# Kernel tuning notes

Hardware: AMD Instinct MI355X
Metric: run time of the kernel (lower is better)

The kernel has to match this reference:

```python
import jax, jax.numpy as jnp
import numpy as np

B, N, D = 16, 1024, 768
H = 12
HS = D // H
L = 2  # n_ffn_layers
EPS = 1e-6


def layernorm(x, scale, bias):
    mu = jnp.mean(x, axis=-1, keepdims=True)
    var = jnp.var(x, axis=-1, keepdims=True)
    return (x - mu) * jax.lax.rsqrt(var + EPS) * scale + bias


def log_cosh(x):
    # numerically stable log(cosh(x)) = |x| + log1p(exp(-2|x|)) - log(2)
    ax = jnp.abs(x)
    return ax + jnp.log1p(jnp.exp(-2.0 * ax)) - jnp.log(2.0)


def setup_inputs() -> dict:
    key = jax.random.key(0)
    ks = jax.random.split(key, 8)
    x = jax.random.normal(ks[0], (B, N, D), dtype=jnp.float32)
    # pre-attention LayerNorm params
    ln1_scale = jnp.ones((D,), jnp.float32)
    ln1_bias = jnp.zeros((D,), jnp.float32)
    # per-head value projections [H, D, HS] (Dense, no bias)
    Wv = jax.random.normal(ks[1], (H, D, HS), jnp.float32) / np.sqrt(D)
    # per-head circulant rows alpha_delta [H, N], truncated_normal(stddev=sqrt(1/N))
    alpha = jax.random.truncated_normal(ks[2], -2.0, 2.0, (H, N), jnp.float32) * np.sqrt(1.0 / N)
    # FFN: L layers of Dense(D) + LayerNorm + swish
    Wf = jax.random.normal(ks[3], (L, D, D), jnp.float32) / np.sqrt(D)
    bf = jnp.zeros((L, D), jnp.float32)
    lnf_scale = jnp.ones((L, D), jnp.float32)
    lnf_bias = jnp.zeros((L, D), jnp.float32)
    return {"x": x, "ln1_scale": ln1_scale, "ln1_bias": ln1_bias, "Wv": Wv,
            "alpha": alpha, "Wf": Wf, "bf": bf,
            "lnf_scale": lnf_scale, "lnf_bias": lnf_bias}


def reference(x, ln1_scale, ln1_bias, Wv, alpha, Wf, bf, lnf_scale, lnf_bias):
    b, n, d = x.shape
    h, hs = Wv.shape[0], Wv.shape[2]
    # --- multi-head positional (circulant) attention on LN(x) ---
    xn = layernorm(x, ln1_scale, ln1_bias)
    v = jnp.einsum('bnd,hdk->bhnk', xn, Wv)  # per-head values
    # circulant matrix C[h, i, j] = alpha[h, (i - j) mod n]  (scipy.linalg.circulant)
    idx = (jnp.arange(n)[:, None] - jnp.arange(n)[None, :]) % n  # [n, n]
    C = alpha[:, idx]                                            # [h, n, n]
    y = jnp.einsum('hij,bhjk->bhik', C, v)                       # [b, h, n, hs]
    y = jnp.transpose(y, (0, 2, 1, 3)).reshape(b, n, h * hs)     # concat heads
    x = x + y
    # --- FFN: [Dense(D) -> LayerNorm -> swish] x L ---
    z = x
    for l in range(Wf.shape[0]):
        z = jax.nn.swish(layernorm(z @ Wf[l] + bf[l], lnf_scale[l], lnf_bias[l]))
    return log_cosh(z + x)
```

## Files before the change

### kernel.cpp

```cpp
#include <hip/hip_runtime.h>
#include <cstdint>
#include <cstddef>


typedef __attribute__((ext_vector_type(8))) short bf16x8;
typedef __attribute__((ext_vector_type(4))) float f32x4;
typedef __attribute__((ext_vector_type(4))) unsigned short us4;

__device__ __forceinline__ unsigned short f2bf(float f) {
  unsigned int u = __builtin_bit_cast(unsigned int, f);
  u += 0x7FFFu + ((u >> 16) & 1u);
  return (unsigned short)(u >> 16);
}
__device__ __forceinline__ float bf2f(unsigned short u) {
  return __builtin_bit_cast(float, (unsigned int)u << 16);
}

__device__ __forceinline__ void g2l16(const void* g, void* l) {
  __builtin_amdgcn_global_load_lds(
      (const __attribute__((address_space(1))) unsigned int*)g,
      (__attribute__((address_space(3))) unsigned int*)l,
      16, 0, 0);
}

#define WAITB(n) asm volatile("s_waitcnt vmcnt(" #n ") lgkmcnt(0)\n\ts_barrier" ::: "memory")

__global__ __launch_bounds__(256) void pack_w2t(const float* __restrict__ Wv,
                                                unsigned short* __restrict__ W2t) {
  int o = blockIdx.x * 256 + threadIdx.x;
  int np = o / 768, d = o - np * 768;
  int h = np >> 6, k = np & 63;
  W2t[o] = f2bf(Wv[h * 49152 + d * 64 + k]);
}

__global__ __launch_bounds__(256) void pack_wft(const float* __restrict__ Wf,
                                                unsigned short* __restrict__ Wft) {
  int o = blockIdx.x * 256 + threadIdx.x;
  int l = o / 589824, rem = o - l * 589824;
  int np = rem / 768, d = rem - np * 768;
  Wft[o] = f2bf(Wf[l * 589824 + d * 768 + np]);
}

__device__ __forceinline__ void wave_reduce2(float& s, float& s2) {
#pragma unroll
  for (int off = 32; off > 0; off >>= 1) {
    s += __shfl_down(s, off);
    s2 += __shfl_down(s2, off);
  }
  s = __shfl(s, 0);
  s2 = __shfl(s2, 0);
}

__global__ __launch_bounds__(256) void ln1_kernel(const float* __restrict__ x,
                                                  const float* __restrict__ sc,
                                                  const float* __restrict__ bi,
                                                  unsigned short* __restrict__ out) {
  int row = blockIdx.x * 4 + (threadIdx.x >> 6);
  int lane = threadIdx.x & 63;
  size_t base = (size_t)row * 768;
  float4 v[3];
#pragma unroll
  for (int j = 0; j < 3; ++j) v[j] = *(const float4*)(x + base + lane * 4 + j * 256);
  float s = 0.f, s2 = 0.f;
#pragma unroll
  for (int j = 0; j < 3; ++j) {
    s += v[j].x + v[j].y + v[j].z + v[j].w;
    s2 += v[j].x * v[j].x + v[j].y * v[j].y + v[j].z * v[j].z + v[j].w * v[j].w;
  }
  wave_reduce2(s, s2);
  float mu = s * (1.0f / 768.0f);
  float var = s2 * (1.0f / 768.0f) - mu * mu;
  float r = rsqrtf(var + 1e-6f);
#pragma unroll
  for (int j = 0; j < 3; ++j) {
    int d = lane * 4 + j * 256;
    float4 scv = *(const float4*)(sc + d);
    float4 biv = *(const float4*)(bi + d);
    us4 o;
    o[0] = f2bf((v[j].x - mu) * r * scv.x + biv.x);
    o[1] = f2bf((v[j].y - mu) * r * scv.y + biv.y);
    o[2] = f2bf((v[j].z - mu) * r * scv.z + biv.z);
    o[3] = f2bf((v[j].w - mu) * r * scv.w + biv.w);
    *(us4*)(out + base + d) = o;
  }
}

__global__ __launch_bounds__(256) void lnswish_kernel(const unsigned short* __restrict__ g,
                                                      const float* __restrict__ sc,
                                                      const float* __restrict__ bi,
                                                      unsigned short* __restrict__ out) {
  int row = blockIdx.x * 4 + (threadIdx.x >> 6);
  int lane = threadIdx.x & 63;
  size_t base = (size_t)row * 768;
  float v[3][4];
#pragma unroll
  for (int j = 0; j < 3; ++j) {
    us4 gv = *(const us4*)(g + base + lane * 4 + j * 256);
#pragma unroll
    for (int q = 0; q < 4; ++q) v[j][q] = bf2f(gv[q]);
  }
  float s = 0.f, s2 = 0.f;
#pragma unroll
  for (int j = 0; j < 3; ++j)
#pragma unroll
    for (int q = 0; q < 4; ++q) { s += v[j][q]; s2 += v[j][q] * v[j][q]; }
  wave_reduce2(s, s2);
  float mu = s * (1.0f / 768.0f);
  float var = s2 * (1.0f / 768.0f) - mu * mu;
  float r = rsqrtf(var + 1e-6f);
#pragma unroll
  for (int j = 0; j < 3; ++j) {
    int d = lane * 4 + j * 256;
    float4 scv = *(const float4*)(sc + d);
    float4 biv = *(const float4*)(bi + d);
    const float* scp = &scv.x;
    const float* bip = &biv.x;
    us4 o;
#pragma unroll
    for (int q = 0; q < 4; ++q) {
      float z = (v[j][q] - mu) * r * scp[q] + bip[q];
      o[q] = f2bf(z / (1.0f + __expf(-z)));
    }
    *(us4*)(out + base + d) = o;
  }
}

__global__ __launch_bounds__(256) void final_kernel(const unsigned short* __restrict__ g,
                                                    const float* __restrict__ sc,
                                                    const float* __restrict__ bi,
                                                    const unsigned short* __restrict__ x2,
                                                    float* __restrict__ out) {
  int row = blockIdx.x * 4 + (threadIdx.x >> 6);
  int lane = threadIdx.x & 63;
  size_t base = (size_t)row * 768;
  float v[3][4];
#pragma unroll
  for (int j = 0; j < 3; ++j) {
    us4 gv = *(const us4*)(g + base + lane * 4 + j * 256);
#pragma unroll
    for (int q = 0; q < 4; ++q) v[j][q] = bf2f(gv[q]);
  }
  float s = 0.f, s2 = 0.f;
#pragma unroll
  for (int j = 0; j < 3; ++j)
#pragma unroll
    for (int q = 0; q < 4; ++q) { s += v[j][q]; s2 += v[j][q] * v[j][q]; }
  wave_reduce2(s, s2);
  float mu = s * (1.0f / 768.0f);
  float var = s2 * (1.0f / 768.0f) - mu * mu;
  float r = rsqrtf(var + 1e-6f);
#pragma unroll
  for (int j = 0; j < 3; ++j) {
    int d = lane * 4 + j * 256;
    float4 scv = *(const float4*)(sc + d);
    float4 biv = *(const float4*)(bi + d);
    us4 xv = *(const us4*)(x2 + base + d);
    const float* scp = &scv.x;
    const float* bip = &biv.x;
    float4 o;
    float* op = &o.x;
#pragma unroll
    for (int q = 0; q < 4; ++q) {
      float z = (v[j][q] - mu) * r * scp[q] + bip[q];
      float sw = z / (1.0f + __expf(-z));
      float t = sw + bf2f(xv[q]);
      float ax = fabsf(t);
      op[q] = ax + __logf(1.0f + __expf(-2.0f * ax)) - 0.69314718055994531f;
    }
    *(float4*)(out + base + d) = o;
  }
}

__device__ __forceinline__ void gemm_core(const unsigned short* __restrict__ A,
                                          const unsigned short* __restrict__ Bt,
                                          int K, int m0, int n0,
                                          unsigned short* sA, unsigned short* sB,
                                          f32x4 acc[4][4]) {
  const int tid = threadIdx.x;
  const int wave = tid >> 6, lane = tid & 63;
  const int wm = (wave >> 1) << 6, wn = (wave & 1) << 6;
  const int fm = lane & 15, fq = lane >> 4;
  const int r0 = tid >> 2, r1 = r0 + 64;
  const int cg = tid & 3;
  const int cs0 = (cg ^ ((r0 >> 1) & 3)) << 3;
  const int cs1 = (cg ^ ((r1 >> 1) & 3)) << 3;
  const int ld0 = r0 * 32 + (cg << 3);
  const int ld1 = r1 * 32 + (cg << 3);
  const int niter = K >> 5;

#define STAGE(k0v, buf)                                                       \
  {                                                                           \
    unsigned short* dA = sA + (buf) * 4096;                                   \
    unsigned short* dB = sB + (buf) * 4096;                                   \
    g2l16(A + (size_t)(m0 + r0) * K + (k0v) + cs0, dA + ld0);                 \
    g2l16(Bt + (size_t)(n0 + r0) * K + (k0v) + cs0, dB + ld0);                \
    g2l16(A + (size_t)(m0 + r1) * K + (k0v) + cs1, dA + ld1);                 \
    g2l16(Bt + (size_t)(n0 + r1) * K + (k0v) + cs1, dB + ld1);                \
  }
#define GCOMP(bc)                                                             \
  {                                                                           \
    const unsigned short* pA = sA + (bc) * 4096;                              \
    const unsigned short* pB = sB + (bc) * 4096;                              \
    bf16x8 aq[4], bq[4];                                                      \
    _Pragma("unroll") for (int t = 0; t < 4; ++t) {                           \
      int ra = wm + (t << 4) + fm;                                            \
      int rb = wn + (t << 4) + fm;                                            \
      aq[t] = *(const bf16x8*)(pA + (ra << 5) + ((fq ^ ((ra >> 1) & 3)) << 3)); \
      bq[t] = *(const bf16x8*)(pB + (rb << 5) + ((fq ^ ((rb >> 1) & 3)) << 3)); \
    }                                                                         \
    _Pragma("unroll") for (int mt = 0; mt < 4; ++mt)                          \
    _Pragma("unroll") for (int nt = 0; nt < 4; ++nt)                          \
      acc[mt][nt] = __builtin_amdgcn_mfma_f32_16x16x32_bf16(aq[mt], bq[nt],   \
                                                            acc[mt][nt], 0, 0, 0); \
  }

  STAGE(0, 0);
  STAGE(32, 1);
  int bs = 2, bc = 0;
  for (int it = 0; it < niter - 1; ++it) {
    WAITB(4);
    if (it + 2 < niter) {
      STAGE((it + 2) << 5, bs);
      bs = (bs == 2) ? 0 : bs + 1;
    }
    GCOMP(bc);
    bc = (bc == 2) ? 0 : bc + 1;
  }
  WAITB(0);
  GCOMP(bc);
#undef STAGE
}

__device__ __forceinline__ void decode_mn_768(int f, int& m0, int& n0) {
  int xcd = f & 7, s = f >> 3;
  int g = s / 6, bx = s - g * 6;
  m0 = (xcd + g * 8) << 7;
  n0 = bx << 7;
}

__global__ __launch_bounds__(256, 3) void gemm1_kernel(const unsigned short* __restrict__ A,
                                                       const unsigned short* __restrict__ Bt,
                                                       unsigned short* __restrict__ Vt) {
  __shared__ unsigned short sA[3 * 4096];
  __shared__ unsigned short sB[3 * 4096];
  f32x4 acc[4][4] = {};
  int m0, n0;
  decode_mn_768(blockIdx.x, m0, n0);
  gemm_core(A, Bt, 768, m0, n0, sA, sB, acc);
  const int wave = threadIdx.x >> 6, lane = threadIdx.x & 63;
  const int wm = (wave >> 1) << 6, wn = (wave & 1) << 6;
  const int fm = lane & 15, fq = lane >> 4;
#pragma unroll
  for (int mt = 0; mt < 4; ++mt) {
    int rowb = m0 + wm + (mt << 4) + (fq << 2);
    int b = rowb >> 10, n = rowb & 1023;
#pragma unroll
    for (int nt = 0; nt < 4; ++nt) {
      int col = n0 + wn + (nt << 4) + fm;
      int h = col >> 6, ck = col & 63;
      size_t off = ((size_t)h << 20) + (size_t)((b << 6) + ck) * 1024 + n;
      us4 v;
#pragma unroll
      for (int r = 0; r < 4; ++r) v[r] = f2bf(acc[mt][nt][r]);
      *(us4*)(Vt + off) = v;
    }
  }
}

__global__ __launch_bounds__(256, 3) void circ_kernel(const float* __restrict__ alpha,
                                                      const unsigned short* __restrict__ Vt,
                                                      const float* __restrict__ xin,
                                                      unsigned short* __restrict__ x2bf) {
  __shared__ unsigned short sAc[8 * 1168];
  __shared__ unsigned short sB[4 * 4096];
  f32x4 acc[4][4] = {};
  int f = blockIdx.x;
  int xcd = f & 7, s = f >> 3;
  int h = s >> 3, t = s & 7;
  int mr = xcd >> 1, nr = xcd & 1;
  int m0 = ((mr << 1) + (t >> 2)) << 7;
  int n0 = ((nr << 2) + (t & 3)) << 7;

  const int tid = threadIdx.x;
  const int wave = tid >> 6, lane = tid & 63;
  const int wm = (wave >> 1) << 6, wn = (wave & 1) << 6;
  const int fm = lane & 15, fq = lane >> 4;

  const float* ah = alpha + (h << 10);
#pragma unroll
  for (int c = 0; c < 8; ++c)
    for (int u = tid; u < 1160; u += 256)
      sAc[c * 1168 + u] = f2bf(ah[(m0 - 897 - u - c) & 1023]);
  asm volatile("s_waitcnt vmcnt(0)" ::: "memory");

  const unsigned short* Bt = Vt + ((size_t)h << 20);
  const int r0 = tid >> 2, r1 = r0 + 64;
  const int cg = tid & 3;
  const int cs0 = (cg ^ ((r0 >> 1) & 3)) << 3;
  const int cs1 = (cg ^ ((r1 >> 1) & 3)) << 3;
  const int ld0 = r0 * 32 + (cg << 3);
  const int ld1 = r1 * 32 + (cg << 3);

#define STAGEB(k0v, buf)                                                      \
  {                                                                           \
    unsigned short* dB = sB + (buf) * 4096;                                   \
    g2l16(Bt + (size_t)(n0 + r0) * 1024 + (k0v) + cs0, dB + ld0);             \
    g2l16(Bt + (size_t)(n0 + r1) * 1024 + (k0v) + cs1, dB + ld1);             \
  }
#define CCOMP(it)                                                             \
  {                                                                           \
    const unsigned short* pB = sB + ((it) & 3) * 4096;                        \
    int k0v = (it) << 5;                                                      \
    bf16x8 aq[4], bq[4];                                                      \
    _Pragma("unroll") for (int t_ = 0; t_ < 4; ++t_) {                        \
      int rl = wm + (t_ << 4) + fm;                                           \
      int d = k0v + (fq << 3) + 127 - rl;                                     \
      int c = d & 7;                                                          \
      aq[t_] = *(const bf16x8*)(sAc + c * 1168 + (d - c));                    \
      int rb = wn + (t_ << 4) + fm;                                           \
      bq[t_] = *(const bf16x8*)(pB + (rb << 5) + ((fq ^ ((rb >> 1) & 3)) << 3)); \
    }                                                                         \
    _Pragma("unroll") for (int mt = 0; mt < 4; ++mt)                          \
    _Pragma("unroll") for (int nt = 0; nt < 4; ++nt)                          \
      acc[mt][nt] = __builtin_amdgcn_mfma_f32_16x16x32_bf16(aq[mt], bq[nt],   \
                                                            acc[mt][nt], 0, 0, 0); \
  }

  STAGEB(0, 0);
  STAGEB(32, 1);
  STAGEB(64, 2);
  for (int it = 0; it < 30; ++it) {
    WAITB(4);
    if (it < 29) STAGEB((it + 3) << 5, (it + 3) & 3);
    CCOMP(it);
  }
  WAITB(2);
  CCOMP(30);
  WAITB(0);
  CCOMP(31);
#undef STAGEB

#pragma unroll
  for (int mt = 0; mt < 4; ++mt) {
    int ib = m0 + wm + (mt << 4) + (fq << 2);
#pragma unroll
    for (int nt = 0; nt < 4; ++nt) {
      int c = n0 + wn + (nt << 4) + fm;
      int b = c >> 6, k = c & 63;
      size_t off = ((size_t)(b << 10) + ib) * 768 + (h << 6) + k;
#pragma unroll
      for (int r = 0; r < 4; ++r) {
        float val = acc[mt][nt][r] + xin[off + (size_t)r * 768];
        x2bf[off + (size_t)r * 768] = f2bf(val);
      }
    }
  }
}

__global__ __launch_bounds__(256, 3) void gemmf_kernel(const unsigned short* __restrict__ A,
                                                       const unsigned short* __restrict__ Bt,
                                                       const float* __restrict__ bias,
                                                       unsigned short* __restrict__ g) {
  __shared__ unsigned short sA[3 * 4096];
  __shared__ unsigned short sB[3 * 4096];
  f32x4 acc[4][4] = {};
  int m0, n0;
  decode_mn_768(blockIdx.x, m0, n0);
  gemm_core(A, Bt, 768, m0, n0, sA, sB, acc);
  const int wave = threadIdx.x >> 6, lane = threadIdx.x & 63;
  const int wm = (wave >> 1) << 6, wn = (wave & 1) << 6;
  const int fm = lane & 15, fq = lane >> 4;
#pragma unroll
  for (int mt = 0; mt < 4; ++mt) {
    int rowb = m0 + wm + (mt << 4) + (fq << 2);
#pragma unroll
    for (int nt = 0; nt < 4; ++nt) {
      int col = n0 + wn + (nt << 4) + fm;
      float bc = bias[col];
#pragma unroll
      for (int r = 0; r < 4; ++r)
        g[(size_t)(rowb + r) * 768 + col] = f2bf(acc[mt][nt][r] + bc);
    }
  }
}

extern "C" void kernel_launch(void* const* d_in, const int* in_sizes, int n_in,
                              void* d_out, int out_size, void* d_ws, size_t ws_size,
                              hipStream_t stream) {
  const float* x = (const float*)d_in[0];
  const float* ln1_s = (const float*)d_in[1];
  const float* ln1_b = (const float*)d_in[2];
  const float* Wv = (const float*)d_in[3];
  const float* alpha = (const float*)d_in[4];
  const float* Wf = (const float*)d_in[5];
  const float* bf = (const float*)d_in[6];
  const float* lnf_s = (const float*)d_in[7];
  const float* lnf_b = (const float*)d_in[8];
  float* out = (float*)d_out;

  char* ws = (char*)d_ws;
  unsigned short* slotA = (unsigned short*)ws;
  unsigned short* Vt = (unsigned short*)(ws + 25165824);
  unsigned short* gbf = Vt;
  unsigned short* slotX = (unsigned short*)(ws + 50331648);
  unsigned short* W2t = (unsigned short*)(ws + 75497472);
  unsigned short* Wft = (unsigned short*)(ws + 76677120);

  pack_w2t<<<2304, 256, 0, stream>>>(Wv, W2t);
  pack_wft<<<4608, 256, 0, stream>>>(Wf, Wft);

  ln1_kernel<<<4096, 256, 0, stream>>>(x, ln1_s, ln1_b, slotA);
  gemm1_kernel<<<768, 256, 0, stream>>>(slotA, W2t, Vt);
  circ_kernel<<<768, 256, 0, stream>>>(alpha, Vt, x, slotX);
  gemmf_kernel<<<768, 256, 0, stream>>>(slotX, Wft, bf, gbf);
  lnswish_kernel<<<4096, 256, 0, stream>>>(gbf, lnf_s, lnf_b, slotA);
  gemmf_kernel<<<768, 256, 0, stream>>>(slotA, Wft + 589824, bf + 768, gbf);
  final_kernel<<<4096, 256, 0, stream>>>(gbf, lnf_s + 768, lnf_b + 768, slotX, out);
}
```

Measured before the change: 282.6 us.

## Replace 128x128 GEMMs with 256x256-tile eight-wave MFMA GEMM using interleaved schedule

The three dense GEMMs (value projection and both FFN layers) move from 128x128 tiles with 4 waves to a 256x256 tile computed by 512 threads. Each K-step is 64 wide, with two LDS buffers in 128KB of dynamic shared memory. The main loop interleaves LDS fragment loads, partial global-to-LDS staging and MFMA quadrants with s_setprio and fine-grained barriers, to raise arithmetic intensity and hide load latency. The trade-off is that only 192 workgroups are launched, fewer than the CU count, and occupancy is limited by the large LDS footprint.

```diff
diff --git a/kernel.cpp b/kernel.cpp
--- a/kernel.cpp
+++ b/kernel.cpp
@@ -24,6 +24,8 @@
 }
 
 #define WAITB(n) asm volatile("s_waitcnt vmcnt(" #n ") lgkmcnt(0)\n\ts_barrier" ::: "memory")
+#define BARX asm volatile("s_waitcnt lgkmcnt(0)\n\ts_barrier" ::: "memory")
+#define BARV(n) asm volatile("s_waitcnt vmcnt(" #n ") lgkmcnt(0)\n\ts_barrier" ::: "memory")
 
 __global__ __launch_bounds__(256) void pack_w2t(const float* __restrict__ Wv,
                                                 unsigned short* __restrict__ W2t) {
@@ -171,98 +173,174 @@
   }
 }
 
-__device__ __forceinline__ void gemm_core(const unsigned short* __restrict__ A,
-                                          const unsigned short* __restrict__ Bt,
-                                          int K, int m0, int n0,
-                                          unsigned short* sA, unsigned short* sB,
-                                          f32x4 acc[4][4]) {
+template <int K>
+__device__ __forceinline__ void gemm256(const unsigned short* __restrict__ A,
+                                        const unsigned short* __restrict__ Bt,
+                                        int m0, int n0, unsigned short* lds,
+                                        f32x4 acc[8][4]) {
   const int tid = threadIdx.x;
-  const int wave = tid >> 6, lane = tid & 63;
-  const int wm = (wave >> 1) << 6, wn = (wave & 1) << 6;
+  const int lane = tid & 63;
+  const int wid = tid >> 6;
+  const int wm = (wid >> 2) << 6;
+  const int wn = (wid & 3) << 5;
   const int fm = lane & 15, fq = lane >> 4;
-  const int r0 = tid >> 2, r1 = r0 + 64;
-  const int cg = tid & 3;
-  const int cs0 = (cg ^ ((r0 >> 1) & 3)) << 3;
-  const int cs1 = (cg ^ ((r1 >> 1) & 3)) << 3;
-  const int ld0 = r0 * 32 + (cg << 3);
-  const int ld1 = r1 * 32 + (cg << 3);
-  const int niter = K >> 5;
-
-#define STAGE(k0v, buf)                                                       \
-  {                                                                           \
-    unsigned short* dA = sA + (buf) * 4096;                                   \
-    unsigned short* dB = sB + (buf) * 4096;                                   \
-    g2l16(A + (size_t)(m0 + r0) * K + (k0v) + cs0, dA + ld0);                 \
-    g2l16(Bt + (size_t)(n0 + r0) * K + (k0v) + cs0, dB + ld0);                \
-    g2l16(A + (size_t)(m0 + r1) * K + (k0v) + cs1, dA + ld1);                 \
-    g2l16(Bt + (size_t)(n0 + r1) * K + (k0v) + cs1, dB + ld1);                \
-  }
-#define GCOMP(bc)                                                             \
-  {                                                                           \
-    const unsigned short* pA = sA + (bc) * 4096;                              \
-    const unsigned short* pB = sB + (bc) * 4096;                              \
-    bf16x8 aq[4], bq[4];                                                      \
-    _Pragma("unroll") for (int t = 0; t < 4; ++t) {                           \
-      int ra = wm + (t << 4) + fm;                                            \
-      int rb = wn + (t << 4) + fm;                                            \
-      aq[t] = *(const bf16x8*)(pA + (ra << 5) + ((fq ^ ((ra >> 1) & 3)) << 3)); \
-      bq[t] = *(const bf16x8*)(pB + (rb << 5) + ((fq ^ ((rb >> 1) & 3)) << 3)); \
-    }                                                                         \
-    _Pragma("unroll") for (int mt = 0; mt < 4; ++mt)                          \
-    _Pragma("unroll") for (int nt = 0; nt < 4; ++nt)                          \
-      acc[mt][nt] = __builtin_amdgcn_mfma_f32_16x16x32_bf16(aq[mt], bq[nt],   \
-                                                            acc[mt][nt], 0, 0, 0); \
-  }
-
-  STAGE(0, 0);
-  STAGE(32, 1);
-  int bs = 2, bc = 0;
-  for (int it = 0; it < niter - 1; ++it) {
-    WAITB(4);
-    if (it + 2 < niter) {
-      STAGE((it + 2) << 5, bs);
-      bs = (bs == 2) ? 0 : bs + 1;
-    }
-    GCOMP(bc);
-    bc = (bc == 2) ? 0 : bc + 1;
-  }
-  WAITB(0);
-  GCOMP(bc);
-#undef STAGE
-}
-
-__device__ __forceinline__ void decode_mn_768(int f, int& m0, int& n0) {
-  int xcd = f & 7, s = f >> 3;
-  int g = s / 6, bx = s - g * 6;
-  m0 = (xcd + g * 8) << 7;
-  n0 = bx << 7;
-}
-
-__global__ __launch_bounds__(256, 3) void gemm1_kernel(const unsigned short* __restrict__ A,
-                                                       const unsigned short* __restrict__ Bt,
-                                                       unsigned short* __restrict__ Vt) {
-  __shared__ unsigned short sA[3 * 4096];
-  __shared__ unsigned short sB[3 * 4096];
-  f32x4 acc[4][4] = {};
+  const int srow = tid >> 3;
+  const int sslot = (tid & 7) ^ (srow & 7);
+  const size_t abase = (size_t)(m0 + srow) * K + (sslot << 3);
+  const size_t bbase = (size_t)(n0 + srow) * K + (sslot << 3);
+
+  bf16x8 aq[4][2], bq[4][2];
+
+#define STG_A(kt, bb, c)                                                     \
+  g2l16(A + abase + (size_t)((c) << 6) * K + ((kt) << 6),                    \
+        lds + ((bb) << 15) + ((c) << 12) + (tid << 3))
+#define STG_B(kt, bb, c)                                                     \
+  g2l16(Bt + bbase + (size_t)((c) << 6) * K + ((kt) << 6),                   \
+        lds + ((bb) << 15) + 16384 + ((c) << 12) + (tid << 3))
+#define LDA(bb, mh)                                                          \
+  _Pragma("unroll") for (int mt = 0; mt < 4; ++mt) {                         \
+    const unsigned short* p =                                                \
+        lds + ((bb) << 15) + (wm + ((mh) << 7) + (mt << 4) + fm) * 64;       \
+    _Pragma("unroll") for (int kk = 0; kk < 2; ++kk)                         \
+      aq[mt][kk] = *(const bf16x8*)(p + ((((kk << 2) + fq) ^ (fm & 7)) << 3)); \
+  }
+#define LDB(bb, nh)                                                          \
+  _Pragma("unroll") for (int nt = 0; nt < 2; ++nt) {                         \
+    const unsigned short* p = lds + ((bb) << 15) + 16384 +                   \
+                              (wn + ((nh) << 7) + (nt << 4) + fm) * 64;      \
+    _Pragma("unroll") for (int kk = 0; kk < 2; ++kk)                         \
+      bq[((nh) << 1) + nt][kk] =                                             \
+          *(const bf16x8*)(p + ((((kk << 2) + fq) ^ (fm & 7)) << 3));        \
+  }
+#define MMX(mh, nh)                                                          \
+  {                                                                          \
+    __builtin_amdgcn_s_setprio(1);                                           \
+    _Pragma("unroll") for (int mt = 0; mt < 4; ++mt)                         \
+    _Pragma("unroll") for (int nt = 0; nt < 2; ++nt)                         \
+    _Pragma("unroll") for (int kk = 0; kk < 2; ++kk)                         \
+      acc[((mh) << 2) + mt][((nh) << 1) + nt] =                              \
+          __builtin_amdgcn_mfma_f32_16x16x32_bf16(                           \
+              aq[mt][kk], bq[((nh) << 1) + nt][kk],                          \
+              acc[((mh) << 2) + mt][((nh) << 1) + nt], 0, 0, 0);             \
+    __builtin_amdgcn_s_setprio(0);                                           \
+  }
+
+  constexpr int NT = K >> 6;
+  STG_A(0, 0, 0); STG_A(0, 0, 1); STG_A(0, 0, 2); STG_A(0, 0, 3);
+  STG_B(0, 0, 0); STG_B(0, 0, 1); STG_B(0, 0, 2); STG_B(0, 0, 3);
+  STG_A(1, 1, 0); STG_A(1, 1, 1);
+  STG_B(1, 1, 0); STG_B(1, 1, 1);
+  BARV(4);
+
+  for (int t = 0; t < (NT >> 1) - 1; ++t) {
+    const int k1 = 2 * t + 1, k2 = 2 * t + 2, k3 = 2 * t + 3;
+    LDA(0, 0); LDB(0, 0);
+    STG_A(k1, 1, 2); STG_A(k1, 1, 3);
+    MMX(0, 0); BARX;
+    LDB(0, 1);
+    STG_B(k1, 1, 2); STG_B(k1, 1, 3);
+    MMX(0, 1); BARX;
+    LDA(0, 1);
+    STG_A(k2, 0, 0); STG_A(k2, 0, 1);
+    MMX(1, 0); BARX;
+    STG_B(k2, 0, 0); STG_B(k2, 0, 1);
+    MMX(1, 1); BARV(4);
+    LDA(1, 0); LDB(1, 0);
+    STG_A(k2, 0, 2); STG_A(k2, 0, 3);
+    MMX(0, 0); BARX;
+    LDB(1, 1);
+    STG_B(k2, 0, 2); STG_B(k2, 0, 3);
+    MMX(0, 1); BARX;
+    LDA(1, 1);
+    STG_A(k3, 1, 0); STG_A(k3, 1, 1);
+    MMX(1, 0); BARX;
+    STG_B(k3, 1, 0); STG_B(k3, 1, 1);
+    MMX(1, 1); BARV(4);
+  }
+  {
+    const int k1 = NT - 1;
+    LDA(0, 0); LDB(0, 0);
+    STG_A(k1, 1, 2); STG_A(k1, 1, 3);
+    MMX(0, 0); BARX;
+    LDB(0, 1);
+    STG_B(k1, 1, 2); STG_B(k1, 1, 3);
+    MMX(0, 1); BARX;
+    LDA(0, 1);
+    MMX(1, 0); BARX;
+    MMX(1, 1);
+    BARV(0);
+    LDA(1, 0); LDB(1, 0);
+    MMX(0, 0); BARX;
+    LDB(1, 1);
+    MMX(0, 1); BARX;
+    LDA(1, 1);
+    MMX(1, 0); BARX;
+    MMX(1, 1);
+  }
+#undef STG_A
+#undef STG_B
+#undef LDA
+#undef LDB
+#undef MMX
+}
+
+__device__ __forceinline__ void decode256(int bid, int& m0, int& n0) {
+  int wg = (bid & 7) * 24 + (bid >> 3);
+  int mi = wg / 3, ni = wg - mi * 3;
+  m0 = mi << 8;
+  n0 = ni << 8;
+}
+
+__global__ __launch_bounds__(512, 2) void gemm1_256(const unsigned short* __restrict__ A,
+                                                    const unsigned short* __restrict__ W2t,
+                                                    unsigned short* __restrict__ Vt) {
+  extern __shared__ unsigned short lds[];
+  f32x4 acc[8][4] = {};
   int m0, n0;
-  decode_mn_768(blockIdx.x, m0, n0);
-  gemm_core(A, Bt, 768, m0, n0, sA, sB, acc);
-  const int wave = threadIdx.x >> 6, lane = threadIdx.x & 63;
-  const int wm = (wave >> 1) << 6, wn = (wave & 1) << 6;
+  decode256(blockIdx.x, m0, n0);
+  gemm256<768>(A, W2t, m0, n0, lds, acc);
+  const int lane = threadIdx.x & 63, wid = threadIdx.x >> 6;
+  const int wm = (wid >> 2) << 6, wn = (wid & 3) << 5;
   const int fm = lane & 15, fq = lane >> 4;
 #pragma unroll
-  for (int mt = 0; mt < 4; ++mt) {
-    int rowb = m0 + wm + (mt << 4) + (fq << 2);
+  for (int ai = 0; ai < 8; ++ai) {
+    int rowb = m0 + wm + ((ai >> 2) << 7) + ((ai & 3) << 4) + (fq << 2);
     int b = rowb >> 10, n = rowb & 1023;
 #pragma unroll
-    for (int nt = 0; nt < 4; ++nt) {
-      int col = n0 + wn + (nt << 4) + fm;
+    for (int nj = 0; nj < 4; ++nj) {
+      int col = n0 + wn + ((nj >> 1) << 7) + ((nj & 1) << 4) + fm;
       int h = col >> 6, ck = col & 63;
       size_t off = ((size_t)h << 20) + (size_t)((b << 6) + ck) * 1024 + n;
       us4 v;
 #pragma unroll
-      for (int r = 0; r < 4; ++r) v[r] = f2bf(acc[mt][nt][r]);
+      for (int r = 0; r < 4; ++r) v[r] = f2bf(acc[ai][nj][r]);
       *(us4*)(Vt + off) = v;
+    }
+  }
+}
+
+__global__ __launch_bounds__(512, 2) void gemmf_256(const unsigned short* __restrict__ A,
+                                                    const unsigned short* __restrict__ Bt,
+                                                    const float* __restrict__ bias,
+                                                    unsigned short* __restrict__ g) {
+  extern __shared__ unsigned short lds[];
+  f32x4 acc[8][4] = {};
+  int m0, n0;
+  decode256(blockIdx.x, m0, n0);
+  gemm256<768>(A, Bt, m0, n0, lds, acc);
+  const int lane = threadIdx.x & 63, wid = threadIdx.x >> 6;
+  const int wm = (wid >> 2) << 6, wn = (wid & 3) << 5;
+  const int fm = lane & 15, fq = lane >> 4;
+#pragma unroll
+  for (int ai = 0; ai < 8; ++ai) {
+    int rowb = m0 + wm + ((ai >> 2) << 7) + ((ai & 3) << 4) + (fq << 2);
+#pragma unroll
+    for (int nj = 0; nj < 4; ++nj) {
+      int col = n0 + wn + ((nj >> 1) << 7) + ((nj & 1) << 4) + fm;
+      float bc = bias[col];
+#pragma unroll
+      for (int r = 0; r < 4; ++r)
+        g[(size_t)(rowb + r) * 768 + col] = f2bf(acc[ai][nj][r] + bc);
     }
   }
 }
@@ -357,33 +435,6 @@
   }
 }
 
-__global__ __launch_bounds__(256, 3) void gemmf_kernel(const unsigned short* __restrict__ A,
-                                                       const unsigned short* __restrict__ Bt,
-                                                       const float* __restrict__ bias,
-                                                       unsigned short* __restrict__ g) {
-  __shared__ unsigned short sA[3 * 4096];
-  __shared__ unsigned short sB[3 * 4096];
-  f32x4 acc[4][4] = {};
-  int m0, n0;
-  decode_mn_768(blockIdx.x, m0, n0);
-  gemm_core(A, Bt, 768, m0, n0, sA, sB, acc);
-  const int wave = threadIdx.x >> 6, lane = threadIdx.x & 63;
-  const int wm = (wave >> 1) << 6, wn = (wave & 1) << 6;
-  const int fm = lane & 15, fq = lane >> 4;
-#pragma unroll
-  for (int mt = 0; mt < 4; ++mt) {
-    int rowb = m0 + wm + (mt << 4) + (fq << 2);
-#pragma unroll
-    for (int nt = 0; nt < 4; ++nt) {
-      int col = n0 + wn + (nt << 4) + fm;
-      float bc = bias[col];
-#pragma unroll
-      for (int r = 0; r < 4; ++r)
-        g[(size_t)(rowb + r) * 768 + col] = f2bf(acc[mt][nt][r] + bc);
-    }
-  }
-}
-
 extern "C" void kernel_launch(void* const* d_in, const int* in_sizes, int n_in,
                               void* d_out, int out_size, void* d_ws, size_t ws_size,
                               hipStream_t stream) {
@@ -406,14 +457,19 @@
   unsigned short* W2t = (unsigned short*)(ws + 75497472);
   unsigned short* Wft = (unsigned short*)(ws + 76677120);
 
+  hipFuncSetAttribute((const void*)gemm1_256,
+                      hipFuncAttributeMaxDynamicSharedMemorySize, 131072);
+  hipFuncSetAttribute((const void*)gemmf_256,
+                      hipFuncAttributeMaxDynamicSharedMemorySize, 131072);
+
   pack_w2t<<<2304, 256, 0, stream>>>(Wv, W2t);
   pack_wft<<<4608, 256, 0, stream>>>(Wf, Wft);
 
   ln1_kernel<<<4096, 256, 0, stream>>>(x, ln1_s, ln1_b, slotA);
-  gemm1_kernel<<<768, 256, 0, stream>>>(slotA, W2t, Vt);
+  gemm1_256<<<192, 512, 131072, stream>>>(slotA, W2t, Vt);
   circ_kernel<<<768, 256, 0, stream>>>(alpha, Vt, x, slotX);
-  gemmf_kernel<<<768, 256, 0, stream>>>(slotX, Wft, bf, gbf);
+  gemmf_256<<<192, 512, 131072, stream>>>(slotX, Wft, bf, gbf);
   lnswish_kernel<<<4096, 256, 0, stream>>>(gbf, lnf_s, lnf_b, slotA);
-  gemmf_kernel<<<768, 256, 0, stream>>>(slotA, Wft + 589824, bf + 768, gbf);
+  gemmf_256<<<192, 512, 131072, stream>>>(slotA, Wft + 589824, bf + 768, gbf);
   final_kernel<<<4096, 256, 0, stream>>>(gbf, lnf_s + 768, lnf_b + 768, slotX, out);
 }
```

Result: no change. 278.4 us (-1.5%).

## Deepen GEMM prefetch pipeline to four LDS stages and merge weight pack kernels

Applied to the files above, without the earlier changes.

The shared GEMM core moves from a triple-buffered to a quad-buffered LDS pipeline with three tiles in flight. The wait count and ring indexing change to match, and gemm1 and gemmf grow their shared buffers and drop launch bounds occupancy from 3 to 2. The two weight-packing kernels are also merged into one launch to save a kernel launch. Deeper prefetch should hide more global latency, but it costs more LDS and lowers occupancy per CU.

```diff
diff --git a/kernel.cpp b/kernel.cpp
--- a/kernel.cpp
+++ b/kernel.cpp
@@ -25,20 +25,22 @@
 
 #define WAITB(n) asm volatile("s_waitcnt vmcnt(" #n ") lgkmcnt(0)\n\ts_barrier" ::: "memory")
 
-__global__ __launch_bounds__(256) void pack_w2t(const float* __restrict__ Wv,
-                                                unsigned short* __restrict__ W2t) {
-  int o = blockIdx.x * 256 + threadIdx.x;
-  int np = o / 768, d = o - np * 768;
-  int h = np >> 6, k = np & 63;
-  W2t[o] = f2bf(Wv[h * 49152 + d * 64 + k]);
-}
-
-__global__ __launch_bounds__(256) void pack_wft(const float* __restrict__ Wf,
+__global__ __launch_bounds__(256) void pack_all(const float* __restrict__ Wv,
+                                                const float* __restrict__ Wf,
+                                                unsigned short* __restrict__ W2t,
                                                 unsigned short* __restrict__ Wft) {
-  int o = blockIdx.x * 256 + threadIdx.x;
-  int l = o / 589824, rem = o - l * 589824;
-  int np = rem / 768, d = rem - np * 768;
-  Wft[o] = f2bf(Wf[l * 589824 + d * 768 + np]);
+  int bid = blockIdx.x;
+  if (bid < 2304) {
+    int o = bid * 256 + threadIdx.x;
+    int np = o / 768, d = o - np * 768;
+    int h = np >> 6, k = np & 63;
+    W2t[o] = f2bf(Wv[h * 49152 + d * 64 + k]);
+  } else {
+    int o = (bid - 2304) * 256 + threadIdx.x;
+    int l = o / 589824, rem = o - l * 589824;
+    int np = rem / 768, d = rem - np * 768;
+    Wft[o] = f2bf(Wf[l * 589824 + d * 768 + np]);
+  }
 }
 
 __device__ __forceinline__ void wave_reduce2(float& s, float& s2) {
@@ -216,19 +218,18 @@
 
   STAGE(0, 0);
   STAGE(32, 1);
-  int bs = 2, bc = 0;
-  for (int it = 0; it < niter - 1; ++it) {
-    WAITB(4);
-    if (it + 2 < niter) {
-      STAGE((it + 2) << 5, bs);
-      bs = (bs == 2) ? 0 : bs + 1;
-    }
-    GCOMP(bc);
-    bc = (bc == 2) ? 0 : bc + 1;
-  }
+  STAGE(64, 2);
+  for (int it = 0; it < niter - 2; ++it) {
+    WAITB(8);
+    if (it + 3 < niter) STAGE((it + 3) << 5, (it + 3) & 3);
+    GCOMP(it & 3);
+  }
+  WAITB(4);
+  GCOMP((niter - 2) & 3);
   WAITB(0);
-  GCOMP(bc);
+  GCOMP((niter - 1) & 3);
 #undef STAGE
+#undef GCOMP
 }
 
 __device__ __forceinline__ void decode_mn_768(int f, int& m0, int& n0) {
@@ -238,11 +239,11 @@
   n0 = bx << 7;
 }
 
-__global__ __launch_bounds__(256, 3) void gemm1_kernel(const unsigned short* __restrict__ A,
+__global__ __launch_bounds__(256, 2) void gemm1_kernel(const unsigned short* __restrict__ A,
                                                        const unsigned short* __restrict__ Bt,
                                                        unsigned short* __restrict__ Vt) {
-  __shared__ unsigned short sA[3 * 4096];
-  __shared__ unsigned short sB[3 * 4096];
+  __shared__ unsigned short sA[4 * 4096];
+  __shared__ unsigned short sB[4 * 4096];
   f32x4 acc[4][4] = {};
   int m0, n0;
   decode_mn_768(blockIdx.x, m0, n0);
@@ -263,6 +264,33 @@
 #pragma unroll
       for (int r = 0; r < 4; ++r) v[r] = f2bf(acc[mt][nt][r]);
       *(us4*)(Vt + off) = v;
+    }
+  }
+}
+
+__global__ __launch_bounds__(256, 2) void gemmf_kernel(const unsigned short* __restrict__ A,
+                                                       const unsigned short* __restrict__ Bt,
+                                                       const float* __restrict__ bias,
+                                                       unsigned short* __restrict__ g) {
+  __shared__ unsigned short sA[4 * 4096];
+  __shared__ unsigned short sB[4 * 4096];
+  f32x4 acc[4][4] = {};
+  int m0, n0;
+  decode_mn_768(blockIdx.x, m0, n0);
+  gemm_core(A, Bt, 768, m0, n0, sA, sB, acc);
+  const int wave = threadIdx.x >> 6, lane = threadIdx.x & 63;
+  const int wm = (wave >> 1) << 6, wn = (wave & 1) << 6;
+  const int fm = lane & 15, fq = lane >> 4;
+#pragma unroll
+  for (int mt = 0; mt < 4; ++mt) {
+    int rowb = m0 + wm + (mt << 4) + (fq << 2);
+#pragma unroll
+    for (int nt = 0; nt < 4; ++nt) {
+      int col = n0 + wn + (nt << 4) + fm;
+      float bc = bias[col];
+#pragma unroll
+      for (int r = 0; r < 4; ++r)
+        g[(size_t)(rowb + r) * 768 + col] = f2bf(acc[mt][nt][r] + bc);
     }
   }
 }
@@ -357,33 +385,6 @@
   }
 }
 
-__global__ __launch_bounds__(256, 3) void gemmf_kernel(const unsigned short* __restrict__ A,
-                                                       const unsigned short* __restrict__ Bt,
-                                                       const float* __restrict__ bias,
-                                                       unsigned short* __restrict__ g) {
-  __shared__ unsigned short sA[3 * 4096];
-  __shared__ unsigned short sB[3 * 4096];
-  f32x4 acc[4][4] = {};
-  int m0, n0;
-  decode_mn_768(blockIdx.x, m0, n0);
-  gemm_core(A, Bt, 768, m0, n0, sA, sB, acc);
-  const int wave = threadIdx.x >> 6, lane = threadIdx.x & 63;
-  const int wm = (wave >> 1) << 6, wn = (wave & 1) << 6;
-  const int fm = lane & 15, fq = lane >> 4;
-#pragma unroll
-  for (int mt = 0; mt < 4; ++mt) {
-    int rowb = m0 + wm + (mt << 4) + (fq << 2);
-#pragma unroll
-    for (int nt = 0; nt < 4; ++nt) {
-      int col = n0 + wn + (nt << 4) + fm;
-      float bc = bias[col];
-#pragma unroll
-      for (int r = 0; r < 4; ++r)
-        g[(size_t)(rowb + r) * 768 + col] = f2bf(acc[mt][nt][r] + bc);
-    }
-  }
-}
-
 extern "C" void kernel_launch(void* const* d_in, const int* in_sizes, int n_in,
                               void* d_out, int out_size, void* d_ws, size_t ws_size,
                               hipStream_t stream) {
@@ -406,8 +407,7 @@
   unsigned short* W2t = (unsigned short*)(ws + 75497472);
   unsigned short* Wft = (unsigned short*)(ws + 76677120);
 
-  pack_w2t<<<2304, 256, 0, stream>>>(Wv, W2t);
-  pack_wft<<<4608, 256, 0, stream>>>(Wf, Wft);
+  pack_all<<<6912, 256, 0, stream>>>(Wv, Wf, W2t, Wft);
 
   ln1_kernel<<<4096, 256, 0, stream>>>(x, ln1_s, ln1_b, slotA);
   gemm1_kernel<<<768, 256, 0, stream>>>(slotA, W2t, Vt);
```

Result: slower. 297.2 us (+5.2%).
